# Optimization experiments

Measured on AMD Instinct MI355X. Metric: run time of the kernel, lower is better.

The kernel has to match this reference:

```python
import jax, jax.numpy as jnp
import numpy as np

SEQLEN, K, OLDK, HEADS = 2048, 1024, 1024, 16
BASE = 10000.0


def rope(x):
    # x: [b, t, K]; RoPENd over 1 channel dim: rotate adjacent pairs
    # pair j at position t rotated by angle t * BASE**(-j/(K/2))
    t = x.shape[1]
    half = K // 2
    theta = 1.0 / (BASE ** (jnp.arange(half, dtype=jnp.float32) / half))  # [half]
    ang = jnp.arange(t, dtype=jnp.float32)[:, None] * theta[None, :]      # [t, half]
    cos, sin = jnp.cos(ang), jnp.sin(ang)
    xr = x.reshape(x.shape[0], t, half, 2)
    xe, xo = xr[..., 0], xr[..., 1]
    re = xe * cos - xo * sin
    im = xe * sin + xo * cos
    return jnp.stack([re, im], axis=-1).reshape(x.shape)


def setup_inputs() -> dict:
    key = jax.random.key(0)
    ks = jax.random.split(key, 5)
    b = 4
    x = jax.random.normal(ks[0], (b, SEQLEN, OLDK), jnp.float32)
    sc_in = 1.0 / np.sqrt(OLDK).astype(np.float32)
    Wq = jax.random.normal(ks[1], (K, OLDK), jnp.float32) * sc_in
    Wk = jax.random.normal(ks[2], (K, OLDK), jnp.float32) * sc_in
    Wv = jax.random.normal(ks[3], (K, OLDK), jnp.float32) * sc_in
    Wu = jax.random.normal(ks[4], (K, K), jnp.float32) * (1.0 / np.sqrt(K).astype(np.float32))
    bu = jnp.zeros((K,), jnp.float32)
    return {"x": x, "Wq": Wq, "Wk": Wk, "Wv": Wv, "Wu": Wu, "bu": bu}


def reference(x, Wq, Wk, Wv, Wu, bu):
    b, t, _ = x.shape
    h = HEADS
    s = K // h  # head dim
    q = rope(x @ Wq.T)   # [b, t, K]
    k = rope(x @ Wk.T)
    v = x @ Wv.T
    # split heads: [b, h, t, s]
    q = q.reshape(b, t, h, s).transpose(0, 2, 1, 3)
    k = k.reshape(b, t, h, s).transpose(0, 2, 1, 3)
    v = v.reshape(b, t, h, s).transpose(0, 2, 1, 3)
    dot = jnp.einsum('bhqd,bhkd->bhqk', q, k) / jnp.sqrt(jnp.float32(s))
    att = jax.nn.softmax(dot, axis=-1)
    out = jnp.einsum('bhqk,bhkd->bhqd', att, v)
    out = out.transpose(0, 2, 1, 3).reshape(b, t, h * s)
    return out @ Wu.T + bu
```

## Files before the change

### kernel.cpp

```cpp
#include <hip/hip_runtime.h>

#define TSEQ 2048
#define KDIM 1024
#define NHEAD 16
#define HDIM 64
#define BATCH 4
#define HALF 512

typedef __attribute__((ext_vector_type(4))) float f32x4;
typedef __attribute__((ext_vector_type(16))) float f32x16;
typedef __attribute__((ext_vector_type(8))) short short8;
typedef __attribute__((ext_vector_type(4))) unsigned short us4;
typedef __attribute__((ext_vector_type(4))) unsigned int u32x4;

#if __has_builtin(__builtin_amdgcn_exp2f)
#define EXP2(x) __builtin_amdgcn_exp2f(x)
#else
#define EXP2(x) __expf((x)*0.6931471805599453f)
#endif

__device__ __forceinline__ unsigned short f2bf(float f){
  unsigned int u = __float_as_uint(f);
  u += 0x7FFFu + ((u >> 16) & 1u);
  return (unsigned short)(u >> 16);
}

__device__ __forceinline__ unsigned int cvtpk(float a, float b){
  unsigned int r;
  asm("v_cvt_pk_bf16_f32 %0, %1, %2" : "=v"(r) : "v"(a), "v"(b));
  return r;
}

__device__ __forceinline__ f32x4 mfma16(short8 a, short8 b, f32x4 c){
  return __builtin_amdgcn_mfma_f32_16x16x32_bf16(a, b, c, 0, 0, 0);
}
__device__ __forceinline__ f32x16 mfma32(short8 a, short8 b, f32x16 c){
  return __builtin_amdgcn_mfma_f32_32x32x16_bf16(a, b, c, 0, 0, 0);
}

__device__ __forceinline__ void gl_lds16(const void* g, void* l){
  __builtin_amdgcn_global_load_lds(
      (const __attribute__((address_space(1))) unsigned int*)g,
      (__attribute__((address_space(3))) unsigned int*)l, 16, 0, 0);
}

__global__ __launch_bounds__(256) void cvt_bf16(const float* __restrict__ in,
                                                unsigned short* __restrict__ out,
                                                int n4){
  int i = blockIdx.x*256 + threadIdx.x;
  if (i >= n4) return;
  f32x4 v = ((const f32x4*)in)[i];
  us4 o;
  o[0] = f2bf(v[0]); o[1] = f2bf(v[1]); o[2] = f2bf(v[2]); o[3] = f2bf(v[3]);
  ((us4*)out)[i] = o;
}

__global__ __launch_bounds__(256) void trig_init(float* __restrict__ cosT,
                                                 float* __restrict__ sinT){
  int idx = blockIdx.x*256 + threadIdx.x;
  int t = idx >> 9;
  int j = idx & (HALF-1);
  float theta = powf(10000.0f, -(float)j * (1.0f/(float)HALF));
  float ang = (float)t * theta;
  cosT[idx] = cosf(ang);
  sinT[idx] = sinf(ang);
}

__global__ __launch_bounds__(256) void gemm_qkv(
    const unsigned short* __restrict__ A,
    const unsigned short* __restrict__ Wq,
    const unsigned short* __restrict__ Wk,
    const unsigned short* __restrict__ Wv,
    unsigned short* __restrict__ Qo,
    unsigned short* __restrict__ Ko,
    unsigned short* __restrict__ Vo,
    const float* __restrict__ cosT,
    const float* __restrict__ sinT){
  __shared__ __align__(16) unsigned short As[128*32];
  __shared__ __align__(16) unsigned short Bs[128*32];
  const int lin = blockIdx.y*64 + blockIdx.x;
  const int swz = (lin & 7)*192 + (lin >> 3);
  const int bx = swz & 63, by = swz >> 6;
  const int region = by >> 3;
  const int tm = bx*128, tn = (by & 7)*128;
  const unsigned short* Bw = region==0 ? Wq : (region==1 ? Wk : Wv);
  unsigned short* outp     = region==0 ? Qo : (region==1 ? Ko : Vo);
  const float scale = (region==0) ? 0.18033688011112042f : 1.0f;

  const int t  = threadIdx.x;
  const int w  = t>>6, l = t&63;
  const int wm = (w>>1)*64, wn = (w&1)*64;
  const int lr = l&15, lk = (l>>4)*8, g4 = (l>>4)*4;

  f32x4 acc[4][4];
  #pragma unroll
  for (int i=0;i<4;i++)
    #pragma unroll
    for (int j=0;j<4;j++) acc[i][j] = (f32x4){0.f,0.f,0.f,0.f};

  const int sr = t>>2, sc = (t&3)*8;
  const unsigned short* Ag = A  + (size_t)(tm+sr)*KDIM + sc;
  const unsigned short* Bg = Bw + (size_t)(tn+sr)*KDIM + sc;
  unsigned short* Al0 = As + t*8;
  unsigned short* Al1 = As + 2048 + t*8;
  unsigned short* Bl0 = Bs + t*8;
  unsigned short* Bl1 = Bs + 2048 + t*8;

  for (int k0=0; k0<KDIM; k0+=32){
    gl_lds16(Ag + k0, Al0);
    gl_lds16(Ag + (size_t)64*KDIM + k0, Al1);
    gl_lds16(Bg + k0, Bl0);
    gl_lds16(Bg + (size_t)64*KDIM + k0, Bl1);
    __syncthreads();
    short8 af[4], bfr[4];
    #pragma unroll
    for (int i=0;i<4;i++) af[i]  = *(const short8*)&As[(wm+i*16+lr)*32 + lk];
    #pragma unroll
    for (int j=0;j<4;j++) bfr[j] = *(const short8*)&Bs[(wn+j*16+lr)*32 + lk];
    #pragma unroll
    for (int i=0;i<4;i++)
      #pragma unroll
      for (int j=0;j<4;j++)
        acc[i][j] = mfma16(af[i], bfr[j], acc[i][j]);
    __syncthreads();
  }

  #pragma unroll
  for (int i=0;i<4;i++){
    #pragma unroll
    for (int j=0;j<4;j++){
      #pragma unroll
      for (int r=0;r<4;r++){
        int row = tm + wm + i*16 + g4 + r;
        int col = tn + wn + j*16 + lr;
        float v = acc[i][j][r];
        if (region < 2){
          float pv = __shfl_xor(v, 1);
          int tp = row & (TSEQ-1);
          int jj = col >> 1;
          float c = cosT[tp*HALF + jj];
          float s = sinT[tp*HALF + jj];
          float res = (col & 1) ? fmaf(pv, s, v*c)
                                : fmaf(v, c, -(pv*s));
          outp[(size_t)row*KDIM + col] = f2bf(res*scale);
        } else {
          outp[(size_t)row*KDIM + col] = f2bf(v);
        }
      }
    }
  }
}

__global__ __launch_bounds__(256) void gemm_out(
    const unsigned short* __restrict__ A,
    const unsigned short* __restrict__ Bw,
    float* __restrict__ outp,
    const float* __restrict__ bias){
  __shared__ __align__(16) unsigned short As[128*32];
  __shared__ __align__(16) unsigned short Bs[128*32];
  const int t  = threadIdx.x;
  const int tm = blockIdx.x*128, tn = blockIdx.y*128;
  const int w  = t>>6, l = t&63;
  const int wm = (w>>1)*64, wn = (w&1)*64;
  const int lr = l&15, lk = (l>>4)*8, g4 = (l>>4)*4;

  f32x4 acc[4][4];
  #pragma unroll
  for (int i=0;i<4;i++)
    #pragma unroll
    for (int j=0;j<4;j++) acc[i][j] = (f32x4){0.f,0.f,0.f,0.f};

  const int sr = t>>2, sc = (t&3)*8;
  const unsigned short* Ag = A  + (size_t)(tm+sr)*KDIM + sc;
  const unsigned short* Bg = Bw + (size_t)(tn+sr)*KDIM + sc;
  unsigned short* Al0 = As + t*8;
  unsigned short* Al1 = As + 2048 + t*8;
  unsigned short* Bl0 = Bs + t*8;
  unsigned short* Bl1 = Bs + 2048 + t*8;

  for (int k0=0; k0<KDIM; k0+=32){
    gl_lds16(Ag + k0, Al0);
    gl_lds16(Ag + (size_t)64*KDIM + k0, Al1);
    gl_lds16(Bg + k0, Bl0);
    gl_lds16(Bg + (size_t)64*KDIM + k0, Bl1);
    __syncthreads();
    short8 af[4], bfr[4];
    #pragma unroll
    for (int i=0;i<4;i++) af[i]  = *(const short8*)&As[(wm+i*16+lr)*32 + lk];
    #pragma unroll
    for (int j=0;j<4;j++) bfr[j] = *(const short8*)&Bs[(wn+j*16+lr)*32 + lk];
    #pragma unroll
    for (int i=0;i<4;i++)
      #pragma unroll
      for (int j=0;j<4;j++)
        acc[i][j] = mfma16(af[i], bfr[j], acc[i][j]);
    __syncthreads();
  }

  #pragma unroll
  for (int i=0;i<4;i++){
    #pragma unroll
    for (int j=0;j<4;j++){
      #pragma unroll
      for (int r=0;r<4;r++){
        int row = tm + wm + i*16 + g4 + r;
        int col = tn + wn + j*16 + lr;
        outp[(size_t)row*KDIM + col] = acc[i][j][r] + bias[col];
      }
    }
  }
}

__global__ __launch_bounds__(256) void karr(const unsigned short* __restrict__ in,
                                            unsigned short* __restrict__ out){
  const int t = threadIdx.x;
  const int tl = blockIdx.x, h = blockIdx.y, b = blockIdx.z;
  const int ks = t>>6, l = t&63, ln = l&31, h2 = l>>5;
  short8 v = *(const short8*)&in[((size_t)b*TSEQ + tl*32 + ln)*KDIM + h*HDIM + ks*16 + h2*8];
  *(short8*)&out[(((size_t)(b*NHEAD + h)*64 + tl)*2048) + t*8] = v;
}

__global__ __launch_bounds__(256) void varr(const unsigned short* __restrict__ in,
                                            unsigned short* __restrict__ out){
  __shared__ __align__(16) unsigned short tile[32][72];
  const int t = threadIdx.x;
  const int tl = blockIdx.x, h = blockIdx.y, b = blockIdx.z;
  const int r = t>>3, c8 = (t&7)*8;
  short8 v = *(const short8*)&in[((size_t)b*TSEQ + tl*32 + r)*KDIM + h*HDIM + c8];
  *(short8*)&tile[r][c8] = v;
  __syncthreads();
  const int dt = t>>7, ks2 = (t>>6)&1;
  const int l = t&63, ln = l&31, h2 = l>>5;
  const int k0 = ks2*16 + h2*8, d = dt*32 + ln;
  unsigned short tmp[8];
  #pragma unroll
  for (int e=0;e<8;e++) tmp[e] = tile[k0+e][d];
  *(short8*)&out[(((size_t)(b*NHEAD + h)*64 + tl)*2048) + t*8] = *(const short8*)tmp;
}

__global__ __launch_bounds__(256, 4) void flash_attn4(
    const unsigned short* __restrict__ Q,
    const unsigned short* __restrict__ Kf,
    const unsigned short* __restrict__ Vf,
    unsigned short* __restrict__ Out){
  __shared__ __align__(16) unsigned short kv[3*4096];
  __shared__ __align__(16) float lbuf[4][32];
  const int t = threadIdx.x;
  const int w = t>>6, l = t&63;
  const int ln = l&31, h = l>>5;
  const int by = blockIdx.y;
  const int b = by>>4, hh = by&15;
  const int q0 = blockIdx.x*128 + w*32;
  const size_t bT = (size_t)b*TSEQ;
  const int hd0 = hh*HDIM;

  short8 qf[4];
  #pragma unroll
  for (int ks=0; ks<4; ks++)
    qf[ks] = *(const short8*)&Q[(bT + q0 + ln)*KDIM + hd0 + ks*16 + h*8];

  const unsigned short* tbK = Kf + (size_t)(b*NHEAD + hh)*64*2048;
  const unsigned short* tbV = Vf + (size_t)(b*NHEAD + hh)*64*2048;

  unsigned short* pA = kv;
  unsigned short* pB = kv + 4096;
  unsigned short* pC = kv + 8192;

  auto STG = [&](int tt, unsigned short* buf){
    gl_lds16(tbK + (size_t)tt*2048 + w*512 + l*8, buf + w*512);
    gl_lds16(tbV + (size_t)tt*2048 + w*512 + l*8, buf + 2048 + w*512);
  };

  STG(0, pA);
  STG(1, pB);
  asm volatile("s_waitcnt vmcnt(2)" ::: "memory");
  __builtin_amdgcn_s_barrier();

  f32x16 O0, O1;
  #pragma unroll
  for (int r=0;r<16;r++){ O0[r]=0.f; O1[r]=0.f; }
  float lsum = 0.f;

  for (int tt=0; tt<64; ++tt){
    if (tt < 62) STG(tt+2, pC);

    short8 kf0 = *(const short8*)&pA[0*512 + l*8];
    short8 kf1 = *(const short8*)&pA[1*512 + l*8];
    short8 kf2 = *(const short8*)&pA[2*512 + l*8];
    short8 kf3 = *(const short8*)&pA[3*512 + l*8];

    f32x16 S;
    #pragma unroll
    for (int r=0;r<16;r++) S[r]=0.f;
    __builtin_amdgcn_s_setprio(1);
    S = mfma32(kf0, qf[0], S);
    S = mfma32(kf1, qf[1], S);
    S = mfma32(kf2, qf[2], S);
    S = mfma32(kf3, qf[3], S);
    __builtin_amdgcn_s_setprio(0);

    float rs = 0.f;
    #pragma unroll
    for (int r=0;r<16;r++){ S[r] = EXP2(S[r]); rs += S[r]; }
    lsum += rs;

    unsigned int wds[8];
    #pragma unroll
    for (int i=0;i<8;i++) wds[i] = cvtpk(S[2*i], S[2*i+1]);

    unsigned int y0 = __shfl_xor(h ? wds[0] : wds[2], 32);
    unsigned int y1 = __shfl_xor(h ? wds[1] : wds[3], 32);
    unsigned int y2 = __shfl_xor(h ? wds[4] : wds[6], 32);
    unsigned int y3 = __shfl_xor(h ? wds[5] : wds[7], 32);

    u32x4 pw0 = h ? (u32x4){y0, y1, wds[2], wds[3]}
                  : (u32x4){wds[0], wds[1], y0, y1};
    u32x4 pw1 = h ? (u32x4){y2, y3, wds[6], wds[7]}
                  : (u32x4){wds[4], wds[5], y2, y3};
    short8 pa0 = *(short8*)&pw0;
    short8 pa1 = *(short8*)&pw1;

    short8 vf0 = *(const short8*)&pA[2048 + 0*512 + l*8];
    short8 vf1 = *(const short8*)&pA[2048 + 1*512 + l*8];
    short8 vf2 = *(const short8*)&pA[2048 + 2*512 + l*8];
    short8 vf3 = *(const short8*)&pA[2048 + 3*512 + l*8];
    __builtin_amdgcn_s_setprio(1);
    O0 = mfma32(pa0, vf0, O0);
    O0 = mfma32(pa1, vf1, O0);
    O1 = mfma32(pa0, vf2, O1);
    O1 = mfma32(pa1, vf3, O1);
    __builtin_amdgcn_s_setprio(0);

    if (tt < 62){
      asm volatile("s_waitcnt vmcnt(2)" ::: "memory");
    } else {
      asm volatile("s_waitcnt vmcnt(0)" ::: "memory");
    }
    __builtin_amdgcn_s_barrier();

    unsigned short* tp = pA; pA = pB; pB = pC; pC = tp;
  }

  float lfull = lsum + __shfl_xor(lsum, 32);
  float linv = 1.0f / lfull;
  if (h == 0) lbuf[w][ln] = linv;
  __syncthreads();

  #pragma unroll
  for (int g=0; g<4; g++){
    f32x4 lv = *(const f32x4*)&lbuf[w][g*8 + h*4];
    #pragma unroll
    for (int i=0; i<4; i++){
      int r = g*4 + i;
      int row = q0 + g*8 + h*4 + i;
      size_t base = (bT + row)*KDIM + hd0;
      Out[base + ln]      = f2bf(O0[r]*lv[i]);
      Out[base + 32 + ln] = f2bf(O1[r]*lv[i]);
    }
  }
}

extern "C" void kernel_launch(void* const* d_in, const int* in_sizes, int n_in,
                              void* d_out, int out_size, void* d_ws, size_t ws_size,
                              hipStream_t stream){
  (void)in_sizes; (void)n_in; (void)out_size; (void)ws_size;
  const float* x  = (const float*)d_in[0];
  const float* Wq = (const float*)d_in[1];
  const float* Wk = (const float*)d_in[2];
  const float* Wv = (const float*)d_in[3];
  const float* Wu = (const float*)d_in[4];
  const float* bu = (const float*)d_in[5];

  char* ws = (char*)d_ws;
  size_t off = 0;
  auto alloc = [&](size_t bytes){ void* p = ws + off; off += bytes; return p; };
  unsigned short* xb  = (unsigned short*)alloc(16777216);
  unsigned short* qb  = (unsigned short*)alloc(16777216);
  unsigned short* kb  = (unsigned short*)alloc(16777216);
  unsigned short* vb  = (unsigned short*)alloc(16777216);
  unsigned short* kfr = (unsigned short*)alloc(16777216);
  unsigned short* wqb = (unsigned short*)alloc(2097152);
  unsigned short* wkb = (unsigned short*)alloc(2097152);
  unsigned short* wvb = (unsigned short*)alloc(2097152);
  unsigned short* wub = (unsigned short*)alloc(2097152);
  float* cosT = (float*)alloc(4194304);
  float* sinT = (float*)alloc(4194304);
  unsigned short* vfr = kb;
  unsigned short* att = xb;

  cvt_bf16<<<8192, 256, 0, stream>>>(x,  xb,  2097152);
  cvt_bf16<<<1024, 256, 0, stream>>>(Wq, wqb, 262144);
  cvt_bf16<<<1024, 256, 0, stream>>>(Wk, wkb, 262144);
  cvt_bf16<<<1024, 256, 0, stream>>>(Wv, wvb, 262144);
  cvt_bf16<<<1024, 256, 0, stream>>>(Wu, wub, 262144);
  trig_init<<<4096, 256, 0, stream>>>(cosT, sinT);

  gemm_qkv<<<dim3(64,24), 256, 0, stream>>>(xb, wqb, wkb, wvb,
                                            qb, kb, vb, cosT, sinT);

  karr<<<dim3(64,16,4), 256, 0, stream>>>(kb, kfr);
  varr<<<dim3(64,16,4), 256, 0, stream>>>(vb, vfr);
  flash_attn4<<<dim3(16,64), 256, 0, stream>>>(qb, kfr, vfr, att);
  gemm_out<<<dim3(64,8), 256, 0, stream>>>(att, wub, (float*)d_out, bu);
}
```

Before: 358.9 us.

## Swizzle GEMM LDS layout, remap block order, interleave cos/sin table

Applies an XOR swizzle to the 16-byte chunks stored in LDS by global_load_lds, so the MFMA fragment reads in both GEMMs avoid bank conflicts. It also changes the block-index remapping in gemm_qkv so consecutive blocks share A rows across all 24 weight tiles, and adds a grouped remap to gemm_out for better L2 reuse. The RoPE cos and sin tables are merged into one interleaved float2 table, so the epilogue does one load instead of two. The main risk is that the swizzle indices on the global load side and the LDS read side must match exactly.

```diff
diff --git a/kernel.cpp b/kernel.cpp
--- a/kernel.cpp
+++ b/kernel.cpp
@@ -55,15 +55,13 @@
   ((us4*)out)[i] = o;
 }
 
-__global__ __launch_bounds__(256) void trig_init(float* __restrict__ cosT,
-                                                 float* __restrict__ sinT){
+__global__ __launch_bounds__(256) void trig_init(float2* __restrict__ csT){
   int idx = blockIdx.x*256 + threadIdx.x;
   int t = idx >> 9;
   int j = idx & (HALF-1);
   float theta = powf(10000.0f, -(float)j * (1.0f/(float)HALF));
   float ang = (float)t * theta;
-  cosT[idx] = cosf(ang);
-  sinT[idx] = sinf(ang);
+  csT[idx] = make_float2(cosf(ang), sinf(ang));
 }
 
 __global__ __launch_bounds__(256) void gemm_qkv(
@@ -74,13 +72,12 @@
     unsigned short* __restrict__ Qo,
     unsigned short* __restrict__ Ko,
     unsigned short* __restrict__ Vo,
-    const float* __restrict__ cosT,
-    const float* __restrict__ sinT){
+    const float2* __restrict__ csT){
   __shared__ __align__(16) unsigned short As[128*32];
   __shared__ __align__(16) unsigned short Bs[128*32];
   const int lin = blockIdx.y*64 + blockIdx.x;
-  const int swz = (lin & 7)*192 + (lin >> 3);
-  const int bx = swz & 63, by = swz >> 6;
+  const int L = (lin & 7)*192 + (lin >> 3);
+  const int bx = L/24, by = L%24;
   const int region = by >> 3;
   const int tm = bx*128, tn = (by & 7)*128;
   const unsigned short* Bw = region==0 ? Wq : (region==1 ? Wk : Wv);
@@ -90,7 +87,7 @@
   const int t  = threadIdx.x;
   const int w  = t>>6, l = t&63;
   const int wm = (w>>1)*64, wn = (w&1)*64;
-  const int lr = l&15, lk = (l>>4)*8, g4 = (l>>4)*4;
+  const int lr = l&15, g = l>>4, g4 = (l>>4)*4;
 
   f32x4 acc[4][4];
   #pragma unroll
@@ -98,7 +95,8 @@
     #pragma unroll
     for (int j=0;j<4;j++) acc[i][j] = (f32x4){0.f,0.f,0.f,0.f};
 
-  const int sr = t>>2, sc = (t&3)*8;
+  const int sr = t>>2, cc = t&3;
+  const int sc = (cc ^ ((sr>>1)&3))*8;
   const unsigned short* Ag = A  + (size_t)(tm+sr)*KDIM + sc;
   const unsigned short* Bg = Bw + (size_t)(tn+sr)*KDIM + sc;
   unsigned short* Al0 = As + t*8;
@@ -114,9 +112,11 @@
     __syncthreads();
     short8 af[4], bfr[4];
     #pragma unroll
-    for (int i=0;i<4;i++) af[i]  = *(const short8*)&As[(wm+i*16+lr)*32 + lk];
-    #pragma unroll
-    for (int j=0;j<4;j++) bfr[j] = *(const short8*)&Bs[(wn+j*16+lr)*32 + lk];
+    for (int i=0;i<4;i++){
+      int ra = wm+i*16+lr, rb = wn+i*16+lr;
+      af[i]  = *(const short8*)&As[ra*32 + (g ^ ((ra>>1)&3))*8];
+      bfr[i] = *(const short8*)&Bs[rb*32 + (g ^ ((rb>>1)&3))*8];
+    }
     #pragma unroll
     for (int i=0;i<4;i++)
       #pragma unroll
@@ -138,10 +138,9 @@
           float pv = __shfl_xor(v, 1);
           int tp = row & (TSEQ-1);
           int jj = col >> 1;
-          float c = cosT[tp*HALF + jj];
-          float s = sinT[tp*HALF + jj];
-          float res = (col & 1) ? fmaf(pv, s, v*c)
-                                : fmaf(v, c, -(pv*s));
+          float2 cs = csT[tp*HALF + jj];
+          float res = (col & 1) ? fmaf(pv, cs.y, v*cs.x)
+                                : fmaf(v, cs.x, -(pv*cs.y));
           outp[(size_t)row*KDIM + col] = f2bf(res*scale);
         } else {
           outp[(size_t)row*KDIM + col] = f2bf(v);
@@ -158,11 +157,14 @@
     const float* __restrict__ bias){
   __shared__ __align__(16) unsigned short As[128*32];
   __shared__ __align__(16) unsigned short Bs[128*32];
+  const int lin = blockIdx.y*64 + blockIdx.x;
+  const int L = (lin & 7)*64 + (lin >> 3);
+  const int bx = L>>3, by = L&7;
+  const int tm = bx*128, tn = by*128;
   const int t  = threadIdx.x;
-  const int tm = blockIdx.x*128, tn = blockIdx.y*128;
   const int w  = t>>6, l = t&63;
   const int wm = (w>>1)*64, wn = (w&1)*64;
-  const int lr = l&15, lk = (l>>4)*8, g4 = (l>>4)*4;
+  const int lr = l&15, g = l>>4, g4 = (l>>4)*4;
 
   f32x4 acc[4][4];
   #pragma unroll
@@ -170,7 +172,8 @@
     #pragma unroll
     for (int j=0;j<4;j++) acc[i][j] = (f32x4){0.f,0.f,0.f,0.f};
 
-  const int sr = t>>2, sc = (t&3)*8;
+  const int sr = t>>2, cc = t&3;
+  const int sc = (cc ^ ((sr>>1)&3))*8;
   const unsigned short* Ag = A  + (size_t)(tm+sr)*KDIM + sc;
   const unsigned short* Bg = Bw + (size_t)(tn+sr)*KDIM + sc;
   unsigned short* Al0 = As + t*8;
@@ -186,9 +189,11 @@
     __syncthreads();
     short8 af[4], bfr[4];
     #pragma unroll
-    for (int i=0;i<4;i++) af[i]  = *(const short8*)&As[(wm+i*16+lr)*32 + lk];
-    #pragma unroll
-    for (int j=0;j<4;j++) bfr[j] = *(const short8*)&Bs[(wn+j*16+lr)*32 + lk];
+    for (int i=0;i<4;i++){
+      int ra = wm+i*16+lr, rb = wn+i*16+lr;
+      af[i]  = *(const short8*)&As[ra*32 + (g ^ ((ra>>1)&3))*8];
+      bfr[i] = *(const short8*)&Bs[rb*32 + (g ^ ((rb>>1)&3))*8];
+    }
     #pragma unroll
     for (int i=0;i<4;i++)
       #pragma unroll
@@ -347,12 +352,12 @@
   __syncthreads();
 
   #pragma unroll
-  for (int g=0; g<4; g++){
-    f32x4 lv = *(const f32x4*)&lbuf[w][g*8 + h*4];
+  for (int gg=0; gg<4; gg++){
+    f32x4 lv = *(const f32x4*)&lbuf[w][gg*8 + h*4];
     #pragma unroll
     for (int i=0; i<4; i++){
-      int r = g*4 + i;
-      int row = q0 + g*8 + h*4 + i;
+      int r = gg*4 + i;
+      int row = q0 + gg*8 + h*4 + i;
       size_t base = (bT + row)*KDIM + hd0;
       Out[base + ln]      = f2bf(O0[r]*lv[i]);
       Out[base + 32 + ln] = f2bf(O1[r]*lv[i]);
@@ -383,8 +388,7 @@
   unsigned short* wkb = (unsigned short*)alloc(2097152);
   unsigned short* wvb = (unsigned short*)alloc(2097152);
   unsigned short* wub = (unsigned short*)alloc(2097152);
-  float* cosT = (float*)alloc(4194304);
-  float* sinT = (float*)alloc(4194304);
+  float2* csT = (float2*)alloc(8388608);
   unsigned short* vfr = kb;
   unsigned short* att = xb;
 
@@ -393,10 +397,10 @@
   cvt_bf16<<<1024, 256, 0, stream>>>(Wk, wkb, 262144);
   cvt_bf16<<<1024, 256, 0, stream>>>(Wv, wvb, 262144);
   cvt_bf16<<<1024, 256, 0, stream>>>(Wu, wub, 262144);
-  trig_init<<<4096, 256, 0, stream>>>(cosT, sinT);
+  trig_init<<<4096, 256, 0, stream>>>(csT);
 
   gemm_qkv<<<dim3(64,24), 256, 0, stream>>>(xb, wqb, wkb, wvb,
-                                            qb, kb, vb, cosT, sinT);
+                                            qb, kb, vb, csT);
 
   karr<<<dim3(64,16,4), 256, 0, stream>>>(kb, kfr);
   varr<<<dim3(64,16,4), 256, 0, stream>>>(vb, vfr);
```

Measured after the change: 364.5 us. No clear change (+1.6%).
